# Optimization experiments

Measured on AMD Instinct MI355X. Metric: run time of the kernel, lower is better.

## Reference

```python
import jax, jax.numpy as jnp
import numpy as np

DIM = 128
HEADS = 4
WS = 7
SHIFT = 3
MLP_HIDDEN = 512
B, H, W = 8, 112, 112


def _rel_pos_index(ws):
    coords = np.stack(np.meshgrid(np.arange(ws), np.arange(ws), indexing='ij'))  # 2,ws,ws
    flat = coords.reshape(2, -1)  # 2, ws*ws
    rel = (flat[:, :, None] - flat[:, None, :]).transpose(1, 2, 0)  # N,N,2
    rel[:, :, 0] += ws - 1
    rel[:, :, 1] += ws - 1
    rel[:, :, 0] *= 2 * ws - 1
    return rel.sum(-1).astype(np.int32)  # N,N


def setup_inputs() -> dict:
    key = jax.random.key(0)
    ks = jax.random.split(key, 12)
    s = 0.02
    return {
        'x': jax.random.normal(ks[0], (B, DIM, H, W), jnp.float32),
        'norm1_g': jnp.ones((DIM,), jnp.float32),
        'norm1_b': jnp.zeros((DIM,), jnp.float32),
        'qkv_w': jax.random.normal(ks[1], (DIM, 3 * DIM), jnp.float32) * s,
        'qkv_b': jnp.zeros((3 * DIM,), jnp.float32),
        'rel_bias_table': jax.random.normal(ks[2], ((2 * WS - 1) ** 2, HEADS), jnp.float32) * s,
        'rel_index': jnp.asarray(_rel_pos_index(WS)),
        'proj_w': jax.random.normal(ks[3], (DIM, DIM), jnp.float32) * s,
        'proj_b': jnp.zeros((DIM,), jnp.float32),
        'norm2_g': jnp.ones((DIM,), jnp.float32),
        'norm2_b': jnp.zeros((DIM,), jnp.float32),
        'fc1_w': jax.random.normal(ks[4], (DIM, MLP_HIDDEN), jnp.float32) * s,
        'fc1_b': jnp.zeros((MLP_HIDDEN,), jnp.float32),
        'fc2_w': jax.random.normal(ks[5], (MLP_HIDDEN, DIM), jnp.float32) * s,
        'fc2_b': jnp.zeros((DIM,), jnp.float32),
    }


def _ln(x, g, b, eps=1e-5):
    m = jnp.mean(x, axis=-1, keepdims=True)
    v = jnp.var(x, axis=-1, keepdims=True)
    return (x - m) * jax.lax.rsqrt(v + eps) * g + b


def _swin_fwd(x, norm1_g, norm1_b, qkv_w, qkv_b, rel_bias_table, rel_index,
              proj_w, proj_b, norm2_g, norm2_b, fc1_w, fc1_b, fc2_w, fc2_b):
    Bb, C, Hh, Ww = x.shape
    x = x.reshape(Bb, C, Hh * Ww).transpose(0, 2, 1)  # B, L, C
    shortcut = x
    x = _ln(x, norm1_g, norm1_b)
    x = x.reshape(Bb, Hh, Ww, C)
    # H, W are multiples of WS here, so no padding needed (pad_r = pad_b = 0)
    if SHIFT > 0:
        x = jnp.roll(x, (-SHIFT, -SHIFT), axis=(1, 2))
    nH, nW = Hh // WS, Ww // WS
    # window partition -> (num_windows, N, C)
    xw = x.reshape(Bb, nH, WS, nW, WS, C).transpose(0, 1, 3, 2, 4, 5).reshape(-1, WS * WS, C)
    NWIN, N = xw.shape[0], WS * WS
    hd = C // HEADS
    qkv = (xw @ qkv_w + qkv_b).reshape(NWIN, N, 3, HEADS, hd).transpose(2, 0, 3, 1, 4)
    q, k, v = qkv[0], qkv[1], qkv[2]  # each (NWIN, HEADS, N, hd)
    scale = hd ** -0.5
    attn = jnp.einsum('whnd,whmd->whnm', q * scale, k)
    bias = rel_bias_table[rel_index.reshape(-1)].reshape(N, N, HEADS).transpose(2, 0, 1)
    attn = jax.nn.softmax(attn + bias[None], axis=-1)
    out = jnp.einsum('whnm,whmd->whnd', attn, v)  # NWIN, HEADS, N, hd
    out = out.transpose(0, 2, 1, 3).reshape(NWIN, N, C) @ proj_w + proj_b
    # window reverse
    x = out.reshape(Bb, nH, nW, WS, WS, C).transpose(0, 1, 3, 2, 4, 5).reshape(Bb, Hh, Ww, C)
    if SHIFT > 0:
        x = jnp.roll(x, (SHIFT, SHIFT), axis=(1, 2))
    x = x.reshape(Bb, Hh * Ww, C)
    x = shortcut + x
    h = _ln(x, norm2_g, norm2_b)
    h = jax.nn.gelu(h @ fc1_w + fc1_b, approximate=False) @ fc2_w + fc2_b
    x = x + h
    return x.transpose(0, 2, 1).reshape(Bb, C, Hh, Ww)


def reference(x, norm1_g, norm1_b, qkv_w, qkv_b, rel_bias_table, rel_index,
              proj_w, proj_b, norm2_g, norm2_b, fc1_w, fc1_b, fc2_w, fc2_b):
    return _swin_fwd(x, norm1_g, norm1_b, qkv_w, qkv_b, rel_bias_table, rel_index,
                     proj_w, proj_b, norm2_g, norm2_b, fc1_w, fc1_b, fc2_w, fc2_b)
```

## Files before the change

kernel.cpp:

```cpp
#include <hip/hip_runtime.h>
#include <hip/hip_bf16.h>
#include <math.h>

typedef __bf16 bf16;
typedef __bf16 bf16x8 __attribute__((ext_vector_type(8)));
typedef float f32x4 __attribute__((ext_vector_type(4)));

#define MFMA(a,b,c) __builtin_amdgcn_mfma_f32_16x16x32_bf16(a,b,c,0,0,0)

static __device__ __forceinline__ int swz256(int row, int kb){ return row*256 + (kb ^ ((row&7)<<4)); }
static __device__ __forceinline__ int swz128(int row, int kb){ return row*128 + (kb ^ ((row&7)<<4)); }
static __device__ __forceinline__ int swz64 (int row, int kb){ return row*64  + (kb ^ ((row&3)<<4)); }

__global__ void k_pack(const float* __restrict__ W, bf16* __restrict__ outp, int K, int N) {
    int idx = blockIdx.x*256 + threadIdx.x;
    int total = (N >> 4) * (K >> 5) * 64;
    if (idx >= total) return;
    int l = idx & 63, f = idx >> 6;
    int KF = K >> 5;
    int kf = f % KF, nf = f / KF;
    int n = nf*16 + (l & 15), k0 = kf*32 + (l >> 4)*8;
    bf16x8 v;
    for (int j = 0; j < 8; ++j) v[j] = (bf16)W[(size_t)(k0+j)*N + n];
    *(bf16x8*)(outp + (size_t)idx*8) = v;
}

__global__ void k_bias(const float* __restrict__ table, const int* __restrict__ ridx,
                       float* __restrict__ bias49) {
    int idx = blockIdx.x*256 + threadIdx.x;
    if (idx >= 2401) return;
    int ri = ridx[idx];
    for (int h = 0; h < 4; ++h) bias49[h*2401 + idx] = table[ri*4 + h];
}

__global__ void k_zero(uint4* __restrict__ xw4) {
    int idx = blockIdx.x*256 + threadIdx.x;
    if (idx >= 2048*240) return;
    int win = idx / 240, rem = idx - win*240;
    xw4[(size_t)win*1024 + 784 + rem] = make_uint4(0,0,0,0);
}

__global__ void __launch_bounds__(256) k_ln1(const float* __restrict__ x,
                                             const float* __restrict__ g1,
                                             const float* __restrict__ b1,
                                             bf16* __restrict__ xw) {
    __shared__ float T[128*113];
    __shared__ float meanL[112], rstdL[112];
    __shared__ float gL[128], bL[128];
    int tid = threadIdx.x;
    int b = blockIdx.x / 112, h = blockIdx.x - (blockIdx.x/112)*112;
    if (tid < 128) { gL[tid] = g1[tid]; bL[tid] = b1[tid]; }
    const float* xp = x + (size_t)b*128*12544 + h*112;
    for (int e = tid; e < 14336; e += 256) {
        int c = e / 112, w = e - c*112;
        T[c*113 + w] = xp[(size_t)c*12544 + w];
    }
    __syncthreads();
    if (tid < 224) {
        int w = tid >> 1, q = tid & 1;
        float s = 0.f, s2 = 0.f;
        for (int i = 0; i < 64; ++i) { float v = T[(q*64 + i)*113 + w]; s += v; s2 += v*v; }
        s  += __shfl_xor(s, 1, 64);
        s2 += __shfl_xor(s2, 1, 64);
        if (q == 0) {
            float m = s * 0.0078125f;
            float var = s2 * 0.0078125f - m*m;
            meanL[w] = m; rstdL[w] = rsqrtf(var + 1e-5f);
        }
    }
    __syncthreads();
    int hr = h + 109; if (hr >= 112) hr -= 112;
    int wh = hr / 7, nr = hr - wh*7;
    for (int e = tid; e < 14336; e += 256) {
        int w = e >> 7, c = e & 127;
        int wr = w + 109; if (wr >= 112) wr -= 112;
        int wwi = wr / 7, nc = wr - wwi*7;
        int win = b*256 + wh*16 + wwi;
        int n = nr*7 + nc;
        float v = (T[c*113 + w] - meanL[w]) * rstdL[w] * gL[c] + bL[c];
        xw[((size_t)win*64 + n)*128 + c] = (bf16)v;
    }
}

__global__ void __launch_bounds__(256) k_attn(const bf16* __restrict__ xw,
                                              const bf16x8* __restrict__ wqkv,
                                              const float* __restrict__ qkv_b,
                                              const bf16x8* __restrict__ wproj,
                                              const float* __restrict__ proj_b,
                                              const float* __restrict__ bias49,
                                              bf16* __restrict__ x1p) {
    __shared__ char lds[65536];
    const int tid = threadIdx.x;
    const int l = tid & 63, wv = tid >> 6;
    const int win = blockIdx.x;
    const int lrow = l & 15, lk = l >> 4;
    char* Q  = lds + wv*8192;
    char* Kt = lds + wv*8192 + 4096;
    char* P  = lds + wv*8192;
    char* VT = lds + 32768 + wv*4096;
    char* AO = lds + 49152;

    {
        const uint4* src = (const uint4*)(xw + (size_t)win*8192);
        for (int it = 0; it < 4; ++it) {
            int unit = it*256 + tid;
            int row = unit >> 4, s = unit & 15;
            *(uint4*)(AO + swz256(row, s*16)) = src[unit];
        }
    }
    __syncthreads();

    f32x4 qa[4][2], ka[4][2], va[4][2];
    {
        float qb0 = qkv_b[      wv*32 + lrow], qb1 = qkv_b[      wv*32 + 16 + lrow];
        float kb0 = qkv_b[128 + wv*32 + lrow], kb1 = qkv_b[128 + wv*32 + 16 + lrow];
        float vb0 = qkv_b[256 + wv*32 + lrow], vb1 = qkv_b[256 + wv*32 + 16 + lrow];
        for (int mf = 0; mf < 4; ++mf) for (int r = 0; r < 4; ++r) {
            qa[mf][0][r] = qb0; qa[mf][1][r] = qb1;
            ka[mf][0][r] = kb0; ka[mf][1][r] = kb1;
            va[mf][0][r] = vb0; va[mf][1][r] = vb1;
        }
        for (int kk = 0; kk < 4; ++kk) {
            bf16x8 a[4];
            for (int mf = 0; mf < 4; ++mf)
                a[mf] = *(const bf16x8*)(AO + swz256(mf*16 + lrow, kk*64 + lk*16));
            for (int nf2 = 0; nf2 < 2; ++nf2) {
                bf16x8 bq = wqkv[(( (     wv*2 + nf2)*4 + kk)*64) + l];
                bf16x8 bk = wqkv[(( ( 8 + wv*2 + nf2)*4 + kk)*64) + l];
                bf16x8 bv = wqkv[(( (16 + wv*2 + nf2)*4 + kk)*64) + l];
                for (int mf = 0; mf < 4; ++mf) {
                    qa[mf][nf2] = MFMA(a[mf], bq, qa[mf][nf2]);
                    ka[mf][nf2] = MFMA(a[mf], bk, ka[mf][nf2]);
                    va[mf][nf2] = MFMA(a[mf], bv, va[mf][nf2]);
                }
            }
        }
        const float scale = 0.17677669529663687f;
        for (int mf = 0; mf < 4; ++mf) for (int nf2 = 0; nf2 < 2; ++nf2)
            for (int r = 0; r < 4; ++r) {
                int row = mf*16 + lk*4 + r;
                int col = nf2*16 + lrow;
                *(bf16*)(Q  + swz64(row, col*2))  = (bf16)(qa[mf][nf2][r] * scale);
                *(bf16*)(Kt + swz64(row, col*2))  = (bf16)(ka[mf][nf2][r]);
                *(bf16*)(VT + swz128(col, row*2)) = (bf16)(va[mf][nf2][r]);
            }
    }
    __syncthreads();

    f32x4 s[4][4];
    {
        const float* bh = bias49 + wv*2401;
        for (int mf = 0; mf < 4; ++mf) for (int nf = 0; nf < 4; ++nf)
            for (int r = 0; r < 4; ++r) {
                int row = mf*16 + lk*4 + r, col = nf*16 + lrow;
                float bv;
                if (col >= 49) bv = -1e30f;
                else if (row < 49) bv = bh[row*49 + col];
                else bv = 0.f;
                s[mf][nf][r] = bv;
            }
        bf16x8 aq[4], bk4[4];
        for (int mf = 0; mf < 4; ++mf) aq[mf]  = *(const bf16x8*)(Q  + swz64(mf*16 + lrow, lk*16));
        for (int nf = 0; nf < 4; ++nf) bk4[nf] = *(const bf16x8*)(Kt + swz64(nf*16 + lrow, lk*16));
        for (int mf = 0; mf < 4; ++mf) for (int nf = 0; nf < 4; ++nf)
            s[mf][nf] = MFMA(aq[mf], bk4[nf], s[mf][nf]);
    }
    for (int mf = 0; mf < 4; ++mf) for (int r = 0; r < 4; ++r) {
        float mx = -3e38f;
        for (int nf = 0; nf < 4; ++nf) mx = fmaxf(mx, s[mf][nf][r]);
        for (int d = 1; d < 16; d <<= 1) mx = fmaxf(mx, __shfl_xor(mx, d, 64));
        float sum = 0.f;
        for (int nf = 0; nf < 4; ++nf) { float p = __expf(s[mf][nf][r] - mx); s[mf][nf][r] = p; sum += p; }
        for (int d = 1; d < 16; d <<= 1) sum += __shfl_xor(sum, d, 64);
        float inv = 1.0f / sum;
        for (int nf = 0; nf < 4; ++nf) s[mf][nf][r] *= inv;
    }
    for (int mf = 0; mf < 4; ++mf) for (int nf = 0; nf < 4; ++nf)
        for (int r = 0; r < 4; ++r) {
            int row = mf*16 + lk*4 + r, col = nf*16 + lrow;
            *(bf16*)(P + swz128(row, col*2)) = (bf16)(s[mf][nf][r]);
        }

    f32x4 o[4][2];
    for (int mf = 0; mf < 4; ++mf) for (int nf = 0; nf < 2; ++nf)
        for (int r = 0; r < 4; ++r) o[mf][nf][r] = 0.f;
    for (int kf = 0; kf < 2; ++kf) {
        bf16x8 ap[4], bv2[2];
        for (int mf = 0; mf < 4; ++mf)
            ap[mf] = *(const bf16x8*)(P + swz128(mf*16 + lrow, kf*64 + lk*16));
        for (int nf = 0; nf < 2; ++nf)
            bv2[nf] = *(const bf16x8*)(VT + swz128(nf*16 + lrow, kf*64 + lk*16));
        for (int mf = 0; mf < 4; ++mf) for (int nf = 0; nf < 2; ++nf)
            o[mf][nf] = MFMA(ap[mf], bv2[nf], o[mf][nf]);
    }
    for (int mf = 0; mf < 4; ++mf) for (int nf = 0; nf < 2; ++nf)
        for (int r = 0; r < 4; ++r) {
            int row = mf*16 + lk*4 + r, col = wv*32 + nf*16 + lrow;
            *(bf16*)(AO + swz256(row, col*2)) = (bf16)(o[mf][nf][r]);
        }
    __syncthreads();

    f32x4 pr[4][2];
    {
        float pb0 = proj_b[wv*32 + lrow], pb1 = proj_b[wv*32 + 16 + lrow];
        for (int mf = 0; mf < 4; ++mf) for (int r = 0; r < 4; ++r) { pr[mf][0][r] = pb0; pr[mf][1][r] = pb1; }
    }
    for (int kk = 0; kk < 4; ++kk) {
        bf16x8 a[4];
        for (int mf = 0; mf < 4; ++mf)
            a[mf] = *(const bf16x8*)(AO + swz256(mf*16 + lrow, kk*64 + lk*16));
        for (int nf = 0; nf < 2; ++nf) {
            bf16x8 bfr = wproj[(((wv*2 + nf)*4 + kk)*64) + l];
            for (int mf = 0; mf < 4; ++mf) pr[mf][nf] = MFMA(a[mf], bfr, pr[mf][nf]);
        }
    }
    {
        int b_ = win >> 8, wh = (win >> 4) & 15, ww = win & 15;
        for (int mf = 0; mf < 4; ++mf) for (int r = 0; r < 4; ++r) {
            int row = mf*16 + lk*4 + r;
            if (row < 49) {
                int nr = row / 7, nc = row - nr*7;
                int h = wh*7 + nr + 3; if (h >= 112) h -= 112;
                int w = ww*7 + nc + 3; if (w >= 112) w -= 112;
                size_t t = (size_t)b_*12544 + h*112 + w;
                for (int nf = 0; nf < 2; ++nf) {
                    int col = wv*32 + nf*16 + lrow;
                    x1p[t*128 + col] = (bf16)pr[mf][nf][r];
                }
            }
        }
    }
}

__global__ void __launch_bounds__(256) k_mlp(const float* __restrict__ x,
                                             const bf16* __restrict__ x1p,
                                             const float* __restrict__ g2,
                                             const float* __restrict__ b2,
                                             const float* __restrict__ fc1_b,
                                             const float* __restrict__ fc2_b,
                                             const bf16x8* __restrict__ wfc1,
                                             const bf16x8* __restrict__ wfc2,
                                             float* __restrict__ out) {
    __shared__ float T[128*65];
    __shared__ char Hq[16384];
    int tid = threadIdx.x;
    int l = tid & 63, wv = tid >> 6;
    int lrow = l & 15, lk = l >> 4;
    int blk = blockIdx.x;
    int b = blk / 196;
    int l0 = (blk - b*196) * 64;
    const float* xb = x + (size_t)b*128*12544 + l0;
    const bf16* xpb = x1p + ((size_t)b*12544 + l0)*128;

    for (int it = 0; it < 32; ++it) {
        int e = it*256 + tid;
        int c = e >> 6, t = e & 63;
        T[c*65 + t] = xb[(size_t)c*12544 + t];
    }
    __syncthreads();

    bf16x8 xf[4][4];
    for (int mf = 0; mf < 4; ++mf) {
        int t = mf*16 + lrow;
        float s = 0.f, s2 = 0.f;
        for (int kk = 0; kk < 4; ++kk) {
            int c0 = kk*32 + lk*8;
            bf16x8 xpv = *(const bf16x8*)(xpb + t*128 + c0);
            bf16x8 v8;
            for (int j = 0; j < 8; ++j) {
                float v = T[(c0+j)*65 + t] + (float)xpv[j];
                v8[j] = (bf16)v;
                float vr = (float)v8[j];
                s += vr; s2 += vr*vr;
            }
            xf[mf][kk] = v8;
        }
        s  += __shfl_xor(s, 16, 64);  s  += __shfl_xor(s, 32, 64);
        s2 += __shfl_xor(s2, 16, 64); s2 += __shfl_xor(s2, 32, 64);
        float m = s * 0.0078125f;
        float var = s2 * 0.0078125f - m*m;
        float rs = rsqrtf(var + 1e-5f);
        for (int kk = 0; kk < 4; ++kk) {
            int c0 = kk*32 + lk*8;
            float4 gv0 = *(const float4*)(g2 + c0), gv1 = *(const float4*)(g2 + c0 + 4);
            float4 bv0 = *(const float4*)(b2 + c0), bv1 = *(const float4*)(b2 + c0 + 4);
            float gg[8] = {gv0.x,gv0.y,gv0.z,gv0.w,gv1.x,gv1.y,gv1.z,gv1.w};
            float bb[8] = {bv0.x,bv0.y,bv0.z,bv0.w,bv1.x,bv1.y,bv1.z,bv1.w};
            bf16x8 v8 = xf[mf][kk];
            for (int j = 0; j < 8; ++j)
                v8[j] = (bf16)(((float)v8[j] - m) * rs * gg[j] + bb[j]);
            xf[mf][kk] = v8;
        }
    }

    f32x4 acc2[4][2];
    for (int mf = 0; mf < 4; ++mf) for (int nf = 0; nf < 2; ++nf) {
        float bv = fc2_b[wv*32 + nf*16 + lrow];
        for (int r = 0; r < 4; ++r) acc2[mf][nf][r] = bv;
    }
    for (int q = 0; q < 4; ++q) {
        f32x4 acc1[4][2];
        for (int mf = 0; mf < 4; ++mf) for (int nf = 0; nf < 2; ++nf) {
            float bv = fc1_b[q*128 + wv*32 + nf*16 + lrow];
            for (int r = 0; r < 4; ++r) acc1[mf][nf][r] = bv;
        }
        for (int kk = 0; kk < 4; ++kk) {
            for (int nf = 0; nf < 2; ++nf) {
                int nfg = q*8 + wv*2 + nf;
                bf16x8 bw = wfc1[(nfg*4 + kk)*64 + l];
                for (int mf = 0; mf < 4; ++mf)
                    acc1[mf][nf] = MFMA(xf[mf][kk], bw, acc1[mf][nf]);
            }
        }
        if (q) __syncthreads();
        for (int mf = 0; mf < 4; ++mf) for (int nf = 0; nf < 2; ++nf)
            for (int r = 0; r < 4; ++r) {
                int row = mf*16 + lk*4 + r, col = wv*32 + nf*16 + lrow;
                float v = acc1[mf][nf][r];
                float u = 0.7978845608f * (v + 0.044715f * v*v*v);
                float e2 = __expf(2.f * u);
                float th = 1.f - 2.f / (e2 + 1.f);
                v = 0.5f * v * (1.f + th);
                *(bf16*)(Hq + swz256(row, col*2)) = (bf16)v;
            }
        __syncthreads();
        for (int kk = 0; kk < 4; ++kk) {
            bf16x8 a[4];
            for (int mf = 0; mf < 4; ++mf)
                a[mf] = *(const bf16x8*)(Hq + swz256(mf*16 + lrow, kk*64 + lk*16));
            for (int nf = 0; nf < 2; ++nf) {
                bf16x8 bw = wfc2[(((wv*2 + nf)*16 + q*4 + kk)*64) + l];
                for (int mf = 0; mf < 4; ++mf)
                    acc2[mf][nf] = MFMA(a[mf], bw, acc2[mf][nf]);
            }
        }
    }

    for (int mf = 0; mf < 4; ++mf) for (int nf = 0; nf < 2; ++nf)
        for (int r = 0; r < 4; ++r) {
            int t = mf*16 + lk*4 + r, c = wv*32 + nf*16 + lrow;
            float v = acc2[mf][nf][r] + T[c*65 + t] + (float)xpb[t*128 + c];
            T[c*65 + t] = v;
        }
    __syncthreads();
    for (int it = 0; it < 32; ++it) {
        int e = it*256 + tid;
        int c = e >> 6, t = e & 63;
        out[(size_t)(b*128 + c)*12544 + l0 + t] = T[c*65 + t];
    }
}

extern "C" void kernel_launch(void* const* d_in, const int* in_sizes, int n_in,
                              void* d_out, int out_size, void* d_ws, size_t ws_size,
                              hipStream_t stream) {
    const float* x      = (const float*)d_in[0];
    const float* n1g    = (const float*)d_in[1];
    const float* n1b    = (const float*)d_in[2];
    const float* qkv_w  = (const float*)d_in[3];
    const float* qkv_b  = (const float*)d_in[4];
    const float* rtab   = (const float*)d_in[5];
    const int*   ridx   = (const int*)  d_in[6];
    const float* proj_w = (const float*)d_in[7];
    const float* proj_b = (const float*)d_in[8];
    const float* n2g    = (const float*)d_in[9];
    const float* n2b    = (const float*)d_in[10];
    const float* fc1_w  = (const float*)d_in[11];
    const float* fc1_b  = (const float*)d_in[12];
    const float* fc2_w  = (const float*)d_in[13];
    const float* fc2_b  = (const float*)d_in[14];
    float* out = (float*)d_out;
    char* ws = (char*)d_ws;

    bf16*  xw     = (bf16*)(ws);
    bf16*  x1p    = (bf16*)(ws + 33554432);
    bf16*  wqkv   = (bf16*)(ws + 59244544);
    bf16*  wproj  = (bf16*)(ws + 59342848);
    bf16*  wfc1   = (bf16*)(ws + 59375616);
    bf16*  wfc2   = (bf16*)(ws + 59506688);
    float* bias49 = (float*)(ws + 59637760);

    hipLaunchKernelGGL(k_pack, dim3(24), dim3(256), 0, stream, qkv_w,  wqkv,  128, 384);
    hipLaunchKernelGGL(k_pack, dim3(8),  dim3(256), 0, stream, proj_w, wproj, 128, 128);
    hipLaunchKernelGGL(k_pack, dim3(32), dim3(256), 0, stream, fc1_w,  wfc1,  128, 512);
    hipLaunchKernelGGL(k_pack, dim3(32), dim3(256), 0, stream, fc2_w,  wfc2,  512, 128);
    hipLaunchKernelGGL(k_bias, dim3(10), dim3(256), 0, stream, rtab, ridx, bias49);
    hipLaunchKernelGGL(k_zero, dim3(1920), dim3(256), 0, stream, (uint4*)xw);
    hipLaunchKernelGGL(k_ln1,  dim3(896),  dim3(256), 0, stream, x, n1g, n1b, xw);
    hipLaunchKernelGGL(k_attn, dim3(2048), dim3(256), 0, stream, xw, (const bf16x8*)wqkv,
                       qkv_b, (const bf16x8*)wproj, proj_b, bias49, x1p);
    hipLaunchKernelGGL(k_mlp,  dim3(1568), dim3(256), 0, stream, x, x1p, n2g, n2b,
                       fc1_b, fc2_b, (const bf16x8*)wfc1, (const bf16x8*)wfc2, out);
}
```

Measured before the change: 363.8 us.

## Shrink LDS and register footprint in attention and MLP kernels to raise occupancy

The attention kernel now computes V separately after Q/K, which shortens the live accumulator set, and reuses LDS regions so it needs 48KB instead of 64KB. The MLP kernel drops the 33KB padded fp32 transpose tile. It reads x directly from global memory for the LayerNorm and residual, stages the normalized activations in swizzled LDS instead of registers, and uses a swizzled 32KB tile for the output transpose. Both kernels get launch_bounds(256,4) to target more resident waves. The cost is extra global reads of x, some strided, plus added barriers and extra LDS reads of A fragments per q iteration.

```diff
diff --git a/kernel.cpp b/kernel.cpp
--- a/kernel.cpp
+++ b/kernel.cpp
@@ -82,56 +82,53 @@
     }
 }
 
-__global__ void __launch_bounds__(256) k_attn(const bf16* __restrict__ xw,
+__global__ void __launch_bounds__(256, 4) k_attn(const bf16* __restrict__ xw,
                                               const bf16x8* __restrict__ wqkv,
                                               const float* __restrict__ qkv_b,
                                               const bf16x8* __restrict__ wproj,
                                               const float* __restrict__ proj_b,
                                               const float* __restrict__ bias49,
                                               bf16* __restrict__ x1p) {
-    __shared__ char lds[65536];
+    __shared__ char lds[49152];
     const int tid = threadIdx.x;
     const int l = tid & 63, wv = tid >> 6;
     const int win = blockIdx.x;
     const int lrow = l & 15, lk = l >> 4;
-    char* Q  = lds + wv*8192;
-    char* Kt = lds + wv*8192 + 4096;
-    char* P  = lds + wv*8192;
-    char* VT = lds + 32768 + wv*4096;
-    char* AO = lds + 49152;
+    char* X  = lds;
+    char* VT = lds + wv*4096;
+    char* Q  = lds + 16384 + wv*8192;
+    char* Kt = Q + 4096;
+    char* P  = Q;
+    char* O  = lds + 16384;
 
     {
         const uint4* src = (const uint4*)(xw + (size_t)win*8192);
         for (int it = 0; it < 4; ++it) {
             int unit = it*256 + tid;
             int row = unit >> 4, s = unit & 15;
-            *(uint4*)(AO + swz256(row, s*16)) = src[unit];
-        }
-    }
-    __syncthreads();
-
-    f32x4 qa[4][2], ka[4][2], va[4][2];
-    {
+            *(uint4*)(X + swz256(row, s*16)) = src[unit];
+        }
+    }
+    __syncthreads();
+
+    {
+        f32x4 qa[4][2], ka[4][2];
         float qb0 = qkv_b[      wv*32 + lrow], qb1 = qkv_b[      wv*32 + 16 + lrow];
         float kb0 = qkv_b[128 + wv*32 + lrow], kb1 = qkv_b[128 + wv*32 + 16 + lrow];
-        float vb0 = qkv_b[256 + wv*32 + lrow], vb1 = qkv_b[256 + wv*32 + 16 + lrow];
         for (int mf = 0; mf < 4; ++mf) for (int r = 0; r < 4; ++r) {
             qa[mf][0][r] = qb0; qa[mf][1][r] = qb1;
             ka[mf][0][r] = kb0; ka[mf][1][r] = kb1;
-            va[mf][0][r] = vb0; va[mf][1][r] = vb1;
         }
         for (int kk = 0; kk < 4; ++kk) {
             bf16x8 a[4];
             for (int mf = 0; mf < 4; ++mf)
-                a[mf] = *(const bf16x8*)(AO + swz256(mf*16 + lrow, kk*64 + lk*16));
+                a[mf] = *(const bf16x8*)(X + swz256(mf*16 + lrow, kk*64 + lk*16));
             for (int nf2 = 0; nf2 < 2; ++nf2) {
-                bf16x8 bq = wqkv[(( (     wv*2 + nf2)*4 + kk)*64) + l];
-                bf16x8 bk = wqkv[(( ( 8 + wv*2 + nf2)*4 + kk)*64) + l];
-                bf16x8 bv = wqkv[(( (16 + wv*2 + nf2)*4 + kk)*64) + l];
+                bf16x8 bq = wqkv[(( (    wv*2 + nf2)*4 + kk)*64) + l];
+                bf16x8 bk = wqkv[(( (8 + wv*2 + nf2)*4 + kk)*64) + l];
                 for (int mf = 0; mf < 4; ++mf) {
                     qa[mf][nf2] = MFMA(a[mf], bq, qa[mf][nf2]);
                     ka[mf][nf2] = MFMA(a[mf], bk, ka[mf][nf2]);
-                    va[mf][nf2] = MFMA(a[mf], bv, va[mf][nf2]);
                 }
             }
         }
@@ -140,12 +137,34 @@
             for (int r = 0; r < 4; ++r) {
                 int row = mf*16 + lk*4 + r;
                 int col = nf2*16 + lrow;
-                *(bf16*)(Q  + swz64(row, col*2))  = (bf16)(qa[mf][nf2][r] * scale);
-                *(bf16*)(Kt + swz64(row, col*2))  = (bf16)(ka[mf][nf2][r]);
-                *(bf16*)(VT + swz128(col, row*2)) = (bf16)(va[mf][nf2][r]);
-            }
-    }
-    __syncthreads();
+                *(bf16*)(Q  + swz64(row, col*2)) = (bf16)(qa[mf][nf2][r] * scale);
+                *(bf16*)(Kt + swz64(row, col*2)) = (bf16)(ka[mf][nf2][r]);
+            }
+    }
+    f32x4 va[4][2];
+    {
+        float vb0 = qkv_b[256 + wv*32 + lrow], vb1 = qkv_b[256 + wv*32 + 16 + lrow];
+        for (int mf = 0; mf < 4; ++mf) for (int r = 0; r < 4; ++r) {
+            va[mf][0][r] = vb0; va[mf][1][r] = vb1;
+        }
+        for (int kk = 0; kk < 4; ++kk) {
+            bf16x8 a[4];
+            for (int mf = 0; mf < 4; ++mf)
+                a[mf] = *(const bf16x8*)(X + swz256(mf*16 + lrow, kk*64 + lk*16));
+            for (int nf2 = 0; nf2 < 2; ++nf2) {
+                bf16x8 bv = wqkv[(((16 + wv*2 + nf2)*4 + kk)*64) + l];
+                for (int mf = 0; mf < 4; ++mf)
+                    va[mf][nf2] = MFMA(a[mf], bv, va[mf][nf2]);
+            }
+        }
+    }
+    __syncthreads();
+    for (int mf = 0; mf < 4; ++mf) for (int nf2 = 0; nf2 < 2; ++nf2)
+        for (int r = 0; r < 4; ++r) {
+            int row = mf*16 + lk*4 + r;
+            int col = nf2*16 + lrow;
+            *(bf16*)(VT + swz128(col, row*2)) = (bf16)(va[mf][nf2][r]);
+        }
 
     f32x4 s[4][4];
     {
@@ -193,10 +212,11 @@
         for (int mf = 0; mf < 4; ++mf) for (int nf = 0; nf < 2; ++nf)
             o[mf][nf] = MFMA(ap[mf], bv2[nf], o[mf][nf]);
     }
+    __syncthreads();
     for (int mf = 0; mf < 4; ++mf) for (int nf = 0; nf < 2; ++nf)
         for (int r = 0; r < 4; ++r) {
             int row = mf*16 + lk*4 + r, col = wv*32 + nf*16 + lrow;
-            *(bf16*)(AO + swz256(row, col*2)) = (bf16)(o[mf][nf][r]);
+            *(bf16*)(O + swz256(row, col*2)) = (bf16)(o[mf][nf][r]);
         }
     __syncthreads();
 
@@ -208,7 +228,7 @@
     for (int kk = 0; kk < 4; ++kk) {
         bf16x8 a[4];
         for (int mf = 0; mf < 4; ++mf)
-            a[mf] = *(const bf16x8*)(AO + swz256(mf*16 + lrow, kk*64 + lk*16));
+            a[mf] = *(const bf16x8*)(O + swz256(mf*16 + lrow, kk*64 + lk*16));
         for (int nf = 0; nf < 2; ++nf) {
             bf16x8 bfr = wproj[(((wv*2 + nf)*4 + kk)*64) + l];
             for (int mf = 0; mf < 4; ++mf) pr[mf][nf] = MFMA(a[mf], bfr, pr[mf][nf]);
@@ -232,7 +252,7 @@
     }
 }
 
-__global__ void __launch_bounds__(256) k_mlp(const float* __restrict__ x,
+__global__ void __launch_bounds__(256, 4) k_mlp(const float* __restrict__ x,
                                              const bf16* __restrict__ x1p,
                                              const float* __restrict__ g2,
                                              const float* __restrict__ b2,
@@ -241,8 +261,11 @@
                                              const bf16x8* __restrict__ wfc1,
                                              const bf16x8* __restrict__ wfc2,
                                              float* __restrict__ out) {
-    __shared__ float T[128*65];
-    __shared__ char Hq[16384];
+    __shared__ char lds[32768];
+    char* XN = lds;
+    char* Hq = lds + 16384;
+    char* OT = lds;
+
     int tid = threadIdx.x;
     int l = tid & 63, wv = tid >> 6;
     int lrow = l & 15, lk = l >> 4;
@@ -252,46 +275,41 @@
     const float* xb = x + (size_t)b*128*12544 + l0;
     const bf16* xpb = x1p + ((size_t)b*12544 + l0)*128;
 
-    for (int it = 0; it < 32; ++it) {
-        int e = it*256 + tid;
-        int c = e >> 6, t = e & 63;
-        T[c*65 + t] = xb[(size_t)c*12544 + t];
-    }
-    __syncthreads();
-
-    bf16x8 xf[4][4];
     for (int mf = 0; mf < 4; ++mf) {
         int t = mf*16 + lrow;
+        float xv[4][8];
         float s = 0.f, s2 = 0.f;
+        #pragma unroll
         for (int kk = 0; kk < 4; ++kk) {
             int c0 = kk*32 + lk*8;
             bf16x8 xpv = *(const bf16x8*)(xpb + t*128 + c0);
-            bf16x8 v8;
+            #pragma unroll
             for (int j = 0; j < 8; ++j) {
-                float v = T[(c0+j)*65 + t] + (float)xpv[j];
-                v8[j] = (bf16)v;
-                float vr = (float)v8[j];
-                s += vr; s2 += vr*vr;
-            }
-            xf[mf][kk] = v8;
+                float v = xb[(size_t)(c0+j)*12544 + t] + (float)xpv[j];
+                xv[kk][j] = v;
+                s += v; s2 += v*v;
+            }
         }
         s  += __shfl_xor(s, 16, 64);  s  += __shfl_xor(s, 32, 64);
         s2 += __shfl_xor(s2, 16, 64); s2 += __shfl_xor(s2, 32, 64);
         float m = s * 0.0078125f;
         float var = s2 * 0.0078125f - m*m;
         float rs = rsqrtf(var + 1e-5f);
+        #pragma unroll
         for (int kk = 0; kk < 4; ++kk) {
             int c0 = kk*32 + lk*8;
             float4 gv0 = *(const float4*)(g2 + c0), gv1 = *(const float4*)(g2 + c0 + 4);
             float4 bv0 = *(const float4*)(b2 + c0), bv1 = *(const float4*)(b2 + c0 + 4);
             float gg[8] = {gv0.x,gv0.y,gv0.z,gv0.w,gv1.x,gv1.y,gv1.z,gv1.w};
             float bb[8] = {bv0.x,bv0.y,bv0.z,bv0.w,bv1.x,bv1.y,bv1.z,bv1.w};
-            bf16x8 v8 = xf[mf][kk];
+            bf16x8 v8;
+            #pragma unroll
             for (int j = 0; j < 8; ++j)
-                v8[j] = (bf16)(((float)v8[j] - m) * rs * gg[j] + bb[j]);
-            xf[mf][kk] = v8;
-        }
-    }
+                v8[j] = (bf16)((xv[kk][j] - m) * rs * gg[j] + bb[j]);
+            *(bf16x8*)(XN + swz256(t, kk*64 + lk*16)) = v8;
+        }
+    }
+    __syncthreads();
 
     f32x4 acc2[4][2];
     for (int mf = 0; mf < 4; ++mf) for (int nf = 0; nf < 2; ++nf) {
@@ -305,11 +323,14 @@
             for (int r = 0; r < 4; ++r) acc1[mf][nf][r] = bv;
         }
         for (int kk = 0; kk < 4; ++kk) {
+            bf16x8 a[4];
+            for (int mf = 0; mf < 4; ++mf)
+                a[mf] = *(const bf16x8*)(XN + swz256(mf*16 + lrow, kk*64 + lk*16));
             for (int nf = 0; nf < 2; ++nf) {
                 int nfg = q*8 + wv*2 + nf;
                 bf16x8 bw = wfc1[(nfg*4 + kk)*64 + l];
                 for (int mf = 0; mf < 4; ++mf)
-                    acc1[mf][nf] = MFMA(xf[mf][kk], bw, acc1[mf][nf]);
+                    acc1[mf][nf] = MFMA(a[mf], bw, acc1[mf][nf]);
             }
         }
         if (q) __syncthreads();
@@ -335,18 +356,24 @@
             }
         }
     }
-
-    for (int mf = 0; mf < 4; ++mf) for (int nf = 0; nf < 2; ++nf)
-        for (int r = 0; r < 4; ++r) {
-            int t = mf*16 + lk*4 + r, c = wv*32 + nf*16 + lrow;
-            float v = acc2[mf][nf][r] + T[c*65 + t] + (float)xpb[t*128 + c];
-            T[c*65 + t] = v;
-        }
+    __syncthreads();
+
+    for (int mf = 0; mf < 4; ++mf) for (int nf = 0; nf < 2; ++nf) {
+        int t0 = mf*16 + lk*4, c = wv*32 + nf*16 + lrow;
+        float4 xo = *(const float4*)(xb + (size_t)c*12544 + t0);
+        float xr[4] = {xo.x, xo.y, xo.z, xo.w};
+        f32x4 v4;
+        #pragma unroll
+        for (int r = 0; r < 4; ++r)
+            v4[r] = acc2[mf][nf][r] + xr[r] + (float)xpb[(t0+r)*128 + c];
+        *(f32x4*)(OT + c*256 + ((t0*4) ^ ((c&15)<<4))) = v4;
+    }
     __syncthreads();
     for (int it = 0; it < 32; ++it) {
         int e = it*256 + tid;
         int c = e >> 6, t = e & 63;
-        out[(size_t)(b*128 + c)*12544 + l0 + t] = T[c*65 + t];
+        float v = *(const float*)(OT + c*256 + ((t*4) ^ ((c&15)<<4)));
+        out[(size_t)(b*128 + c)*12544 + l0 + t] = v;
     }
 }
 
```

Result: slower. 392.2 us (+7.8%).
